# Kernel optimization log

Measured on AMD Instinct MI355X. Metric: run time of the kernel, lower is better.

Reference implementation:

```python
import math
import jax, jax.numpy as jnp
import numpy as np

B, T, C, HS = 4, 4096, 2048, 128

def setup_inputs() -> dict:
    key = jax.random.key(0)
    k1, k2, k3, k4 = jax.random.split(key, 4)
    x = jax.random.normal(k1, (B, T, C), dtype=jnp.float32)
    # torch Linear init ~ U(-1/sqrt(in), 1/sqrt(in)); normal*0.02 is fine for a numeric baseline
    Wq = jax.random.normal(k2, (C, HS), dtype=jnp.float32) * 0.02
    Wk = jax.random.normal(k3, (C, HS), dtype=jnp.float32) * 0.02
    Wv = jax.random.normal(k4, (C, HS), dtype=jnp.float32) * 0.02
    return {"x": x, "Wq": Wq, "Wk": Wk, "Wv": Wv}

def reference(x, Wq, Wk, Wv):
    # Single-head causal self-attention (dropout in eval mode = identity).
    q = x @ Wq          # [B,T,HS]
    k = x @ Wk          # [B,T,HS]
    v = x @ Wv          # [B,T,HS]
    scale = 1.0 / math.sqrt(HS)
    att = jnp.einsum('bqd,bkd->bqk', q, k) * scale          # [B,T,T]
    causal = jnp.tril(jnp.ones((T, T), dtype=bool))          # [T,T]
    att = jnp.where(causal[None, :, :], att, -jnp.inf)
    att = jax.nn.softmax(att, axis=-1)
    y = jnp.einsum('bqk,bkd->bqd', att, v)                   # [B,T,HS]
    return y
```

## Files before the change

### kernel.cpp

```cpp
#include <hip/hip_runtime.h>
#include <hip/hip_bf16.h>


#define B_  4
#define T_  4096
#define C_  2048
#define HS_ 128

typedef unsigned short u16;
typedef __attribute__((ext_vector_type(8))) short short8;
typedef __attribute__((ext_vector_type(4))) float floatx4;

static __device__ __forceinline__ u16 f2bf(float x) {
  union { float f; unsigned u; } c; c.f = x;
  unsigned r = 0x7fffu + ((c.u >> 16) & 1u);
  return (u16)((c.u + r) >> 16);
}

__global__ __launch_bounds__(256) void wtrans3_kernel(
    const float* __restrict__ Wq, const float* __restrict__ Wk,
    const float* __restrict__ Wv, u16* __restrict__ dst) {
  __shared__ u16 tile[32][33];
  int z = blockIdx.z;
  const float* src = (z == 0) ? Wq : (z == 1) ? Wk : Wv;
  u16* d = dst + (size_t)z * HS_ * C_;
  int c0 = blockIdx.x * 32, r0 = blockIdx.y * 32;
  int tx = threadIdx.x, ty = threadIdx.y;
#pragma unroll
  for (int i = 0; i < 4; ++i)
    tile[ty + 8 * i][tx] = f2bf(src[(size_t)(r0 + ty + 8 * i) * HS_ + (c0 + tx)]);
  __syncthreads();
#pragma unroll
  for (int i = 0; i < 4; ++i)
    d[(size_t)(c0 + ty + 8 * i) * C_ + (r0 + tx)] = tile[tx][ty + 8 * i];
}

#define GBM 64
#define GBK 64
#define LPAD 72

__global__ __launch_bounds__(256) void qkv_gemm_kernel(
    const float* __restrict__ X, const u16* __restrict__ WT3,
    u16* __restrict__ qkv, u16* __restrict__ vT) {
  __shared__ u16 smem[GBM * LPAD + HS_ * LPAD];
  u16 (*Xs)[LPAD] = (u16(*)[LPAD])smem;
  u16 (*Ws)[LPAD] = (u16(*)[LPAD])(smem + GBM * LPAD);

  int z = blockIdx.y;
  const u16* Wt = WT3 + (size_t)z * HS_ * C_;
  int t = threadIdx.x;
  int wv = t >> 6, lane = t & 63;
  int l15 = lane & 15, hi = lane >> 4;
  int wm = (wv & 1) * 32, wn = (wv >> 1) * 64;
  size_t mbase = (size_t)blockIdx.x * GBM;

  int xm = t >> 3, xc = t & 7;

  const float* xrow0 = &X[(mbase + xm) * C_];
  const float* xrow1 = &X[(mbase + 32 + xm) * C_];
  const u16* wrow0 = &Wt[(size_t)(xm) * C_];
  const u16* wrow1 = &Wt[(size_t)(32 + xm) * C_];
  const u16* wrow2 = &Wt[(size_t)(64 + xm) * C_];
  const u16* wrow3 = &Wt[(size_t)(96 + xm) * C_];

  floatx4 acc[2][4];
#pragma unroll
  for (int i = 0; i < 2; ++i)
#pragma unroll
    for (int j = 0; j < 4; ++j) acc[i][j] = (floatx4){0.f, 0.f, 0.f, 0.f};

  floatx4 xreg[2][2];
  short8 wreg[4];
  {
    int koff = xc * 8;
    xreg[0][0] = *(const floatx4*)&xrow0[koff];
    xreg[0][1] = *(const floatx4*)&xrow0[koff + 4];
    xreg[1][0] = *(const floatx4*)&xrow1[koff];
    xreg[1][1] = *(const floatx4*)&xrow1[koff + 4];
    wreg[0] = *(const short8*)&wrow0[koff];
    wreg[1] = *(const short8*)&wrow1[koff];
    wreg[2] = *(const short8*)&wrow2[koff];
    wreg[3] = *(const short8*)&wrow3[koff];
  }

  for (int kt = 0; kt < C_ / GBK; ++kt) {
#pragma unroll
    for (int i = 0; i < 2; ++i) {
      short8 v;
#pragma unroll
      for (int j = 0; j < 4; ++j) {
        v[j] = (short)f2bf(xreg[i][0][j]);
        v[4 + j] = (short)f2bf(xreg[i][1][j]);
      }
      *(short8*)&Xs[i * 32 + xm][xc * 8] = v;
    }
    *(short8*)&Ws[xm][xc * 8] = wreg[0];
    *(short8*)&Ws[32 + xm][xc * 8] = wreg[1];
    *(short8*)&Ws[64 + xm][xc * 8] = wreg[2];
    *(short8*)&Ws[96 + xm][xc * 8] = wreg[3];
    __syncthreads();

    if (kt + 1 < C_ / GBK) {
      int koff = (kt + 1) * GBK + xc * 8;
      xreg[0][0] = *(const floatx4*)&xrow0[koff];
      xreg[0][1] = *(const floatx4*)&xrow0[koff + 4];
      xreg[1][0] = *(const floatx4*)&xrow1[koff];
      xreg[1][1] = *(const floatx4*)&xrow1[koff + 4];
      wreg[0] = *(const short8*)&wrow0[koff];
      wreg[1] = *(const short8*)&wrow1[koff];
      wreg[2] = *(const short8*)&wrow2[koff];
      wreg[3] = *(const short8*)&wrow3[koff];
    }

#pragma unroll
    for (int ks = 0; ks < 2; ++ks) {
      short8 af[2], bf[4];
#pragma unroll
      for (int mt = 0; mt < 2; ++mt)
        af[mt] = *(const short8*)&Xs[wm + mt * 16 + l15][ks * 32 + hi * 8];
#pragma unroll
      for (int nt = 0; nt < 4; ++nt)
        bf[nt] = *(const short8*)&Ws[wn + nt * 16 + l15][ks * 32 + hi * 8];
#pragma unroll
      for (int mt = 0; mt < 2; ++mt)
#pragma unroll
        for (int nt = 0; nt < 4; ++nt)
          acc[mt][nt] = __builtin_amdgcn_mfma_f32_16x16x32_bf16(
              af[mt], bf[nt], acc[mt][nt], 0, 0, 0);
    }
    __syncthreads();
  }

  if (z != 2) {
    u16* outp = qkv + (size_t)z * ((size_t)B_ * T_ * HS_);
#pragma unroll
    for (int mt = 0; mt < 2; ++mt)
#pragma unroll
      for (int nt = 0; nt < 4; ++nt)
#pragma unroll
        for (int r = 0; r < 4; ++r) {
          size_t row = mbase + wm + mt * 16 + hi * 4 + r;
          int col = wn + nt * 16 + l15;
          outp[row * HS_ + col] = f2bf(acc[mt][nt][r]);
        }
  } else {
    u16 (*Tb)[LPAD] = (u16(*)[LPAD])smem;
#pragma unroll
    for (int mt = 0; mt < 2; ++mt)
#pragma unroll
      for (int nt = 0; nt < 4; ++nt)
#pragma unroll
        for (int r = 0; r < 4; ++r)
          Tb[wn + nt * 16 + l15][wm + mt * 16 + hi * 4 + r] = f2bf(acc[mt][nt][r]);
    __syncthreads();
    int b = (int)(mbase >> 12);
    int trow0 = (int)(mbase & (T_ - 1));
    u16* vb = vT + (size_t)b * HS_ * T_;
#pragma unroll
    for (int i = 0; i < 4; ++i) {
      int id = i * 256 + t;
      int c = id >> 3, ch = id & 7;
      short8 v = *(const short8*)&Tb[c][ch * 8];
      *(short8*)&vb[(size_t)c * T_ + trow0 + ch * 8] = v;
    }
  }
}

#define BQ 64
#define BKV 64
#define CHUNK 16

template <bool WRITE_PARTIAL>
static __device__ __forceinline__ void flash_body(
    const u16* __restrict__ q, const u16* __restrict__ k,
    const u16* __restrict__ vT, float* __restrict__ outO,
    float* __restrict__ Mp, float* __restrict__ Lp,
    int b, int qb, int kb0, int kb1, int slot) {
  __shared__ u16 Ks[BKV][136];
  __shared__ u16 Vs[144][72];
  __shared__ u16 Ps[BQ][72];
  int t = threadIdx.x;
  int wv = t >> 6, lane = t & 63, l15 = lane & 15, hi = lane >> 4;

  const float sc = 0.08838834764831845f * 1.4426950408889634f;

  short8 qf[4];
  {
    const u16* qrow = q + (size_t)(b * T_ + qb * BQ + wv * 16 + l15) * HS_;
#pragma unroll
    for (int ks = 0; ks < 4; ++ks)
      qf[ks] = *(const short8*)(qrow + ks * 32 + hi * 8);
  }

  {
    int r = 128 + (t >> 4), c0 = (t & 15) * 4;
    const u16 one = 0x3F80;
    Vs[r][c0] = one; Vs[r][c0 + 1] = one;
    Vs[r][c0 + 2] = one; Vs[r][c0 + 3] = one;
  }

  floatx4 of[9];
#pragma unroll
  for (int dt = 0; dt < 9; ++dt) of[dt] = (floatx4){0.f, 0.f, 0.f, 0.f};
  float m_run[4];
#pragma unroll
  for (int r = 0; r < 4; ++r) m_run[r] = -__builtin_inff();

  const u16* kbase = k + (size_t)b * T_ * HS_;
  const u16* vbase = vT + (size_t)b * HS_ * T_;

  short8 kreg[4], vreg[4];
#pragma unroll
  for (int i = 0; i < 4; ++i) {
    int id = i * 256 + t;
    int n = id >> 4, ck = id & 15;
    kreg[i] = *(const short8*)&kbase[(size_t)(kb0 * BKV + n) * HS_ + ck * 8];
    int d = id >> 3, cv = id & 7;
    vreg[i] = *(const short8*)&vbase[(size_t)d * T_ + kb0 * BKV + cv * 8];
  }

  for (int kb = kb0; kb <= kb1; ++kb) {
#pragma unroll
    for (int i = 0; i < 4; ++i) {
      int id = i * 256 + t;
      int n = id >> 4, ck = id & 15;
      *(short8*)&Ks[n][ck * 8] = kreg[i];
      int d = id >> 3, cv = id & 7;
      *(short8*)&Vs[d][cv * 8] = vreg[i];
    }
    __syncthreads();

    if (kb < kb1) {
#pragma unroll
      for (int i = 0; i < 4; ++i) {
        int id = i * 256 + t;
        int n = id >> 4, ck = id & 15;
        kreg[i] = *(const short8*)&kbase[(size_t)((kb + 1) * BKV + n) * HS_ + ck * 8];
        int d = id >> 3, cv = id & 7;
        vreg[i] = *(const short8*)&vbase[(size_t)d * T_ + (kb + 1) * BKV + cv * 8];
      }
    }

    floatx4 sf[4];
#pragma unroll
    for (int nt = 0; nt < 4; ++nt) {
      floatx4 s = (floatx4){0.f, 0.f, 0.f, 0.f};
#pragma unroll
      for (int ks = 0; ks < 4; ++ks) {
        short8 bfrag = *(const short8*)&Ks[nt * 16 + l15][ks * 32 + hi * 8];
        s = __builtin_amdgcn_mfma_f32_16x16x32_bf16(qf[ks], bfrag, s, 0, 0, 0);
      }
      sf[nt] = s;
    }

    float sv[4][4];
    if (kb == qb) {
#pragma unroll
      for (int nt = 0; nt < 4; ++nt) {
        int col = nt * 16 + l15;
#pragma unroll
        for (int r = 0; r < 4; ++r) {
          int row = wv * 16 + hi * 4 + r;
          sv[nt][r] = (col <= row) ? sf[nt][r] * sc : -__builtin_inff();
        }
      }
    } else {
#pragma unroll
      for (int nt = 0; nt < 4; ++nt)
#pragma unroll
        for (int r = 0; r < 4; ++r) sv[nt][r] = sf[nt][r] * sc;
    }

    float mt4[4];
#pragma unroll
    for (int r = 0; r < 4; ++r)
      mt4[r] = fmaxf(fmaxf(sv[0][r], sv[1][r]), fmaxf(sv[2][r], sv[3][r]));
#pragma unroll
    for (int off = 1; off < 16; off <<= 1)
#pragma unroll
      for (int r = 0; r < 4; ++r)
        mt4[r] = fmaxf(mt4[r], __shfl_xor(mt4[r], off));

    bool need = false;
#pragma unroll
    for (int r = 0; r < 4; ++r) need = need || (mt4[r] > m_run[r] + 8.f);
    if (__any(need)) {
      float alpha[4];
#pragma unroll
      for (int r = 0; r < 4; ++r) {
        float mn = fmaxf(m_run[r], mt4[r]);
        alpha[r] = exp2f(m_run[r] - mn);
        m_run[r] = mn;
      }
#pragma unroll
      for (int dt = 0; dt < 9; ++dt)
#pragma unroll
        for (int r = 0; r < 4; ++r) of[dt][r] *= alpha[r];
    }

    float pv[4][4];
#pragma unroll
    for (int nt = 0; nt < 4; ++nt)
#pragma unroll
      for (int r = 0; r < 4; ++r) pv[nt][r] = exp2f(sv[nt][r] - m_run[r]);

#pragma unroll
    for (int nt = 0; nt < 4; ++nt)
#pragma unroll
      for (int r = 0; r < 4; ++r)
        Ps[wv * 16 + hi * 4 + r][nt * 16 + l15] = f2bf(pv[nt][r]);
    __asm__ volatile("s_waitcnt lgkmcnt(0)" ::: "memory");

#pragma unroll
    for (int ks2 = 0; ks2 < 2; ++ks2) {
      short8 af = *(const short8*)&Ps[wv * 16 + l15][ks2 * 32 + hi * 8];
#pragma unroll
      for (int dt = 0; dt < 9; ++dt) {
        short8 bfrag = *(const short8*)&Vs[dt * 16 + l15][ks2 * 32 + hi * 8];
        of[dt] = __builtin_amdgcn_mfma_f32_16x16x32_bf16(af, bfrag, of[dt], 0, 0, 0);
      }
    }
    __syncthreads();
  }

  if (WRITE_PARTIAL) {
    float* Op = outO + (size_t)slot * (BQ * HS_);
#pragma unroll
    for (int dt = 0; dt < 8; ++dt)
#pragma unroll
      for (int r = 0; r < 4; ++r) {
        int row = wv * 16 + hi * 4 + r;
        Op[row * HS_ + dt * 16 + l15] = of[dt][r];
      }
    if (l15 == 0) {
#pragma unroll
      for (int r = 0; r < 4; ++r) {
        int row = wv * 16 + hi * 4 + r;
        Mp[slot * BQ + row] = m_run[r];
        Lp[slot * BQ + row] = of[8][r];
      }
    }
  } else {
    float rl[4];
#pragma unroll
    for (int r = 0; r < 4; ++r) rl[r] = 1.0f / of[8][r];
#pragma unroll
    for (int dt = 0; dt < 8; ++dt)
#pragma unroll
      for (int r = 0; r < 4; ++r) {
        size_t row = (size_t)(b * T_ + qb * BQ + wv * 16 + hi * 4 + r);
        outO[row * HS_ + dt * 16 + l15] = of[dt][r] * rl[r];
      }
  }
}

__global__ __launch_bounds__(256, 3) void flash_partial_kernel(
    const u16* __restrict__ q, const u16* __restrict__ k,
    const u16* __restrict__ vT, float* __restrict__ Opart,
    float* __restrict__ Mpart, float* __restrict__ Lpart) {
  int qb = blockIdx.x, c = blockIdx.y, b = blockIdx.z;
  int kb0 = c * CHUNK;
  if (kb0 > qb) return;
  int kb1 = min(qb, kb0 + CHUNK - 1);
  int slot = (b * (T_ / BQ) + qb) * 4 + c;
  flash_body<true>(q, k, vT, Opart, Mpart, Lpart, b, qb, kb0, kb1, slot);
}

__global__ __launch_bounds__(256, 3) void flash_attn_kernel(
    const u16* __restrict__ q, const u16* __restrict__ k,
    const u16* __restrict__ vT, float* __restrict__ out) {
  int qb = blockIdx.x, b = blockIdx.y;
  flash_body<false>(q, k, vT, out, nullptr, nullptr, b, qb, 0, qb, 0);
}

__global__ __launch_bounds__(256) void flash_merge_kernel(
    const float* __restrict__ Opart, const float* __restrict__ Mpart,
    const float* __restrict__ Lpart, float* __restrict__ out) {
  __shared__ float w[4][BQ];
  __shared__ float invL[BQ];
  int qb = blockIdx.x, b = blockIdx.y;
  int t = threadIdx.x;
  int nch = qb / CHUNK + 1;
  int slot0 = (b * (T_ / BQ) + qb) * 4;

  if (t < BQ) {
    float mv[4], mmax = -__builtin_inff();
    for (int c = 0; c < nch; ++c) {
      mv[c] = Mpart[(slot0 + c) * BQ + t];
      mmax = fmaxf(mmax, mv[c]);
    }
    float L = 0.f;
    for (int c = 0; c < nch; ++c) {
      float wc = exp2f(mv[c] - mmax);
      w[c][t] = wc;
      L += wc * Lpart[(slot0 + c) * BQ + t];
    }
    invL[t] = 1.0f / L;
  }
  __syncthreads();

  size_t obase = ((size_t)(b * T_) + (size_t)qb * BQ) * HS_;
#pragma unroll
  for (int j = 0; j < 32; ++j) {
    int e = j * 256 + t;
    int row = e >> 7;
    float acc = 0.f;
    for (int c = 0; c < nch; ++c)
      acc += w[c][row] * Opart[(size_t)(slot0 + c) * (BQ * HS_) + e];
    out[obase + e] = acc * invL[row];
  }
}

extern "C" void kernel_launch(void* const* d_in, const int* in_sizes, int n_in,
                              void* d_out, int out_size, void* d_ws, size_t ws_size,
                              hipStream_t stream) {
  const float* x  = (const float*)d_in[0];
  const float* Wq = (const float*)d_in[1];
  const float* Wk = (const float*)d_in[2];
  const float* Wv = (const float*)d_in[3];
  float* out = (float*)d_out;

  u16* ws = (u16*)d_ws;
  const size_t wtsz  = (size_t)HS_ * C_;
  const size_t qkvsz = (size_t)B_ * T_ * HS_;
  u16* WT = ws;
  u16* qv = WT + 3 * wtsz;
  u16* kv = qv + qkvsz;
  u16* vT = kv + qkvsz;
  const size_t base_bytes = (3 * wtsz + 3 * qkvsz) * sizeof(u16);

  const int NSLOT = B_ * (T_ / BQ) * 4;
  float* Opart = (float*)((char*)d_ws + base_bytes);
  float* Mpart = Opart + (size_t)NSLOT * BQ * HS_;
  float* Lpart = Mpart + (size_t)NSLOT * BQ;
  const size_t split_bytes =
      base_bytes + ((size_t)NSLOT * BQ * HS_ + 2 * (size_t)NSLOT * BQ) * sizeof(float);

  dim3 tb(32, 8);
  wtrans3_kernel<<<dim3(HS_ / 32, C_ / 32, 3), tb, 0, stream>>>(Wq, Wk, Wv, WT);

  qkv_gemm_kernel<<<dim3((B_ * T_) / GBM, 3), 256, 0, stream>>>(x, WT, qv, vT);

  if (ws_size >= split_bytes) {
    flash_partial_kernel<<<dim3(T_ / BQ, 4, B_), 256, 0, stream>>>(
        qv, kv, vT, Opart, Mpart, Lpart);
    flash_merge_kernel<<<dim3(T_ / BQ, B_), 256, 0, stream>>>(
        Opart, Mpart, Lpart, out);
  } else {
    flash_attn_kernel<<<dim3(T_ / BQ, B_), 256, 0, stream>>>(qv, kv, vT, out);
  }
}
```

Before: 306.9 us.

## Fuse Q/K/V projections into one GEMM block with double-buffered LDS

Measured after the change: 322.2 us. 5.0% more time.

```diff
diff --git a/kernel.cpp b/kernel.cpp
--- a/kernel.cpp
+++ b/kernel.cpp
@@ -37,128 +37,137 @@
 
 #define GBM 64
 #define GBK 64
-#define LPAD 72
-
-__global__ __launch_bounds__(256) void qkv_gemm_kernel(
+#define NKT (C_ / GBK)
+
+__global__ __launch_bounds__(512) void qkv_gemm_fused(
     const float* __restrict__ X, const u16* __restrict__ WT3,
     u16* __restrict__ qkv, u16* __restrict__ vT) {
-  __shared__ u16 smem[GBM * LPAD + HS_ * LPAD];
-  u16 (*Xs)[LPAD] = (u16(*)[LPAD])smem;
-  u16 (*Ws)[LPAD] = (u16(*)[LPAD])(smem + GBM * LPAD);
-
-  int z = blockIdx.y;
-  const u16* Wt = WT3 + (size_t)z * HS_ * C_;
+  __shared__ u16 Xs[2][GBM][72];
+  __shared__ u16 Ws[2][3 * HS_][72];
+
   int t = threadIdx.x;
   int wv = t >> 6, lane = t & 63;
   int l15 = lane & 15, hi = lane >> 4;
-  int wm = (wv & 1) * 32, wn = (wv >> 1) * 64;
+  int wm = (wv & 1) * 32;
+  int wn = (wv >> 1) * 32;
   size_t mbase = (size_t)blockIdx.x * GBM;
 
   int xm = t >> 3, xc = t & 7;
-
-  const float* xrow0 = &X[(mbase + xm) * C_];
-  const float* xrow1 = &X[(mbase + 32 + xm) * C_];
-  const u16* wrow0 = &Wt[(size_t)(xm) * C_];
-  const u16* wrow1 = &Wt[(size_t)(32 + xm) * C_];
-  const u16* wrow2 = &Wt[(size_t)(64 + xm) * C_];
-  const u16* wrow3 = &Wt[(size_t)(96 + xm) * C_];
-
-  floatx4 acc[2][4];
-#pragma unroll
-  for (int i = 0; i < 2; ++i)
-#pragma unroll
-    for (int j = 0; j < 4; ++j) acc[i][j] = (floatx4){0.f, 0.f, 0.f, 0.f};
-
-  floatx4 xreg[2][2];
-  short8 wreg[4];
+  const float* xrow = &X[(mbase + xm) * C_];
+  const u16* wb[6];
+#pragma unroll
+  for (int j = 0; j < 6; ++j) {
+    int g = xm + 64 * j;
+    wb[j] = &WT3[(size_t)(g >> 7) * HS_ * C_ + (size_t)(g & 127) * C_];
+  }
+
+  floatx4 acc[3][2][2];
+#pragma unroll
+  for (int z = 0; z < 3; ++z)
+#pragma unroll
+    for (int i = 0; i < 2; ++i)
+#pragma unroll
+      for (int j = 0; j < 2; ++j) acc[z][i][j] = (floatx4){0.f, 0.f, 0.f, 0.f};
+
+  floatx4 xreg[2];
+  short8 wreg[6];
+
   {
     int koff = xc * 8;
-    xreg[0][0] = *(const floatx4*)&xrow0[koff];
-    xreg[0][1] = *(const floatx4*)&xrow0[koff + 4];
-    xreg[1][0] = *(const floatx4*)&xrow1[koff];
-    xreg[1][1] = *(const floatx4*)&xrow1[koff + 4];
-    wreg[0] = *(const short8*)&wrow0[koff];
-    wreg[1] = *(const short8*)&wrow1[koff];
-    wreg[2] = *(const short8*)&wrow2[koff];
-    wreg[3] = *(const short8*)&wrow3[koff];
-  }
-
-  for (int kt = 0; kt < C_ / GBK; ++kt) {
-#pragma unroll
-    for (int i = 0; i < 2; ++i) {
-      short8 v;
+    xreg[0] = *(const floatx4*)&xrow[koff];
+    xreg[1] = *(const floatx4*)&xrow[koff + 4];
+#pragma unroll
+    for (int j = 0; j < 6; ++j) wreg[j] = *(const short8*)&wb[j][koff];
+  }
+  {
+    short8 xv;
+#pragma unroll
+    for (int j = 0; j < 4; ++j) {
+      xv[j] = (short)f2bf(xreg[0][j]);
+      xv[4 + j] = (short)f2bf(xreg[1][j]);
+    }
+    *(short8*)&Xs[0][xm][xc * 8] = xv;
+#pragma unroll
+    for (int j = 0; j < 6; ++j) *(short8*)&Ws[0][xm + 64 * j][xc * 8] = wreg[j];
+  }
+  __syncthreads();
+
+  for (int kt = 0; kt < NKT; ++kt) {
+    int p = kt & 1;
+    if (kt + 1 < NKT) {
+      int koff = (kt + 1) * GBK + xc * 8;
+      xreg[0] = *(const floatx4*)&xrow[koff];
+      xreg[1] = *(const floatx4*)&xrow[koff + 4];
+#pragma unroll
+      for (int j = 0; j < 6; ++j) wreg[j] = *(const short8*)&wb[j][koff];
+    }
+
+#pragma unroll
+    for (int ks = 0; ks < 2; ++ks) {
+      short8 af[2];
+#pragma unroll
+      for (int mt = 0; mt < 2; ++mt)
+        af[mt] = *(const short8*)&Xs[p][wm + mt * 16 + l15][ks * 32 + hi * 8];
+#pragma unroll
+      for (int z = 0; z < 3; ++z)
+#pragma unroll
+        for (int nt = 0; nt < 2; ++nt) {
+          short8 bfrag =
+              *(const short8*)&Ws[p][z * HS_ + wn + nt * 16 + l15][ks * 32 + hi * 8];
+#pragma unroll
+          for (int mt = 0; mt < 2; ++mt)
+            acc[z][mt][nt] = __builtin_amdgcn_mfma_f32_16x16x32_bf16(
+                af[mt], bfrag, acc[z][mt][nt], 0, 0, 0);
+        }
+    }
+
+    if (kt + 1 < NKT) {
+      short8 xv;
 #pragma unroll
       for (int j = 0; j < 4; ++j) {
-        v[j] = (short)f2bf(xreg[i][0][j]);
-        v[4 + j] = (short)f2bf(xreg[i][1][j]);
-      }
-      *(short8*)&Xs[i * 32 + xm][xc * 8] = v;
-    }
-    *(short8*)&Ws[xm][xc * 8] = wreg[0];
-    *(short8*)&Ws[32 + xm][xc * 8] = wreg[1];
-    *(short8*)&Ws[64 + xm][xc * 8] = wreg[2];
-    *(short8*)&Ws[96 + xm][xc * 8] = wreg[3];
+        xv[j] = (short)f2bf(xreg[0][j]);
+        xv[4 + j] = (short)f2bf(xreg[1][j]);
+      }
+      *(short8*)&Xs[p ^ 1][xm][xc * 8] = xv;
+#pragma unroll
+      for (int j = 0; j < 6; ++j)
+        *(short8*)&Ws[p ^ 1][xm + 64 * j][xc * 8] = wreg[j];
+    }
     __syncthreads();
-
-    if (kt + 1 < C_ / GBK) {
-      int koff = (kt + 1) * GBK + xc * 8;
-      xreg[0][0] = *(const floatx4*)&xrow0[koff];
-      xreg[0][1] = *(const floatx4*)&xrow0[koff + 4];
-      xreg[1][0] = *(const floatx4*)&xrow1[koff];
-      xreg[1][1] = *(const floatx4*)&xrow1[koff + 4];
-      wreg[0] = *(const short8*)&wrow0[koff];
-      wreg[1] = *(const short8*)&wrow1[koff];
-      wreg[2] = *(const short8*)&wrow2[koff];
-      wreg[3] = *(const short8*)&wrow3[koff];
-    }
-
-#pragma unroll
-    for (int ks = 0; ks < 2; ++ks) {
-      short8 af[2], bf[4];
-#pragma unroll
-      for (int mt = 0; mt < 2; ++mt)
-        af[mt] = *(const short8*)&Xs[wm + mt * 16 + l15][ks * 32 + hi * 8];
-#pragma unroll
-      for (int nt = 0; nt < 4; ++nt)
-        bf[nt] = *(const short8*)&Ws[wn + nt * 16 + l15][ks * 32 + hi * 8];
-#pragma unroll
-      for (int mt = 0; mt < 2; ++mt)
-#pragma unroll
-        for (int nt = 0; nt < 4; ++nt)
-          acc[mt][nt] = __builtin_amdgcn_mfma_f32_16x16x32_bf16(
-              af[mt], bf[nt], acc[mt][nt], 0, 0, 0);
-    }
-    __syncthreads();
-  }
-
-  if (z != 2) {
-    u16* outp = qkv + (size_t)z * ((size_t)B_ * T_ * HS_);
+  }
+
+  const size_t qkvsz = (size_t)B_ * T_ * HS_;
+#pragma unroll
+  for (int z = 0; z < 2; ++z) {
+    u16* outp = qkv + (size_t)z * qkvsz;
 #pragma unroll
     for (int mt = 0; mt < 2; ++mt)
 #pragma unroll
-      for (int nt = 0; nt < 4; ++nt)
+      for (int nt = 0; nt < 2; ++nt)
 #pragma unroll
         for (int r = 0; r < 4; ++r) {
           size_t row = mbase + wm + mt * 16 + hi * 4 + r;
           int col = wn + nt * 16 + l15;
-          outp[row * HS_ + col] = f2bf(acc[mt][nt][r]);
+          outp[row * HS_ + col] = f2bf(acc[z][mt][nt][r]);
         }
-  } else {
-    u16 (*Tb)[LPAD] = (u16(*)[LPAD])smem;
-#pragma unroll
-    for (int mt = 0; mt < 2; ++mt)
-#pragma unroll
-      for (int nt = 0; nt < 4; ++nt)
-#pragma unroll
-        for (int r = 0; r < 4; ++r)
-          Tb[wn + nt * 16 + l15][wm + mt * 16 + hi * 4 + r] = f2bf(acc[mt][nt][r]);
-    __syncthreads();
+  }
+
+  u16 (*Tb)[72] = (u16(*)[72])Ws[0];
+#pragma unroll
+  for (int mt = 0; mt < 2; ++mt)
+#pragma unroll
+    for (int nt = 0; nt < 2; ++nt)
+#pragma unroll
+      for (int r = 0; r < 4; ++r)
+        Tb[wn + nt * 16 + l15][wm + mt * 16 + hi * 4 + r] = f2bf(acc[2][mt][nt][r]);
+  __syncthreads();
+  {
     int b = (int)(mbase >> 12);
     int trow0 = (int)(mbase & (T_ - 1));
     u16* vb = vT + (size_t)b * HS_ * T_;
 #pragma unroll
-    for (int i = 0; i < 4; ++i) {
-      int id = i * 256 + t;
+    for (int i = 0; i < 2; ++i) {
+      int id = i * 512 + t;
       int c = id >> 3, ch = id & 7;
       short8 v = *(const short8*)&Tb[c][ch * 8];
       *(short8*)&vb[(size_t)c * T_ + trow0 + ch * 8] = v;
@@ -439,7 +448,7 @@
   dim3 tb(32, 8);
   wtrans3_kernel<<<dim3(HS_ / 32, C_ / 32, 3), tb, 0, stream>>>(Wq, Wk, Wv, WT);
 
-  qkv_gemm_kernel<<<dim3((B_ * T_) / GBM, 3), 256, 0, stream>>>(x, WT, qv, vT);
+  qkv_gemm_fused<<<dim3((B_ * T_) / GBM), 512, 0, stream>>>(x, WT, qv, vT);
 
   if (ws_size >= split_bytes) {
     flash_partial_kernel<<<dim3(T_ / BQ, 4, B_), 256, 0, stream>>>(
```

## Double-buffer LDS and enlarge QKV GEMM M-tile to 128 rows

Applied to the files above, without the earlier changes.

After: 322.2 us. 5.0% more time.

```diff
diff --git a/kernel.cpp b/kernel.cpp
--- a/kernel.cpp
+++ b/kernel.cpp
@@ -35,106 +35,117 @@
     d[(size_t)(c0 + ty + 8 * i) * C_ + (r0 + tx)] = tile[tx][ty + 8 * i];
 }
 
-#define GBM 64
+#define GBM 128
 #define GBK 64
-#define LPAD 72
-
-__global__ __launch_bounds__(256) void qkv_gemm_kernel(
+#define NKT (C_ / GBK)
+#define XP 72
+#define TP 136
+
+__global__ __launch_bounds__(256, 2) void qkv_gemm_kernel(
     const float* __restrict__ X, const u16* __restrict__ WT3,
     u16* __restrict__ qkv, u16* __restrict__ vT) {
-  __shared__ u16 smem[GBM * LPAD + HS_ * LPAD];
-  u16 (*Xs)[LPAD] = (u16(*)[LPAD])smem;
-  u16 (*Ws)[LPAD] = (u16(*)[LPAD])(smem + GBM * LPAD);
+  __shared__ u16 smem[2 * 2 * GBM * XP];
+  u16 (*Xs)[GBM][XP] = (u16(*)[GBM][XP])smem;
+  u16 (*Ws)[GBM][XP] = (u16(*)[GBM][XP])(smem + 2 * GBM * XP);
 
   int z = blockIdx.y;
   const u16* Wt = WT3 + (size_t)z * HS_ * C_;
   int t = threadIdx.x;
   int wv = t >> 6, lane = t & 63;
   int l15 = lane & 15, hi = lane >> 4;
-  int wm = (wv & 1) * 32, wn = (wv >> 1) * 64;
+  int wm = (wv & 1) * 64;
+  int wn = (wv >> 1) * 64;
   size_t mbase = (size_t)blockIdx.x * GBM;
 
-  int xm = t >> 3, xc = t & 7;
-
-  const float* xrow0 = &X[(mbase + xm) * C_];
-  const float* xrow1 = &X[(mbase + 32 + xm) * C_];
-  const u16* wrow0 = &Wt[(size_t)(xm) * C_];
-  const u16* wrow1 = &Wt[(size_t)(32 + xm) * C_];
-  const u16* wrow2 = &Wt[(size_t)(64 + xm) * C_];
-  const u16* wrow3 = &Wt[(size_t)(96 + xm) * C_];
-
-  floatx4 acc[2][4];
-#pragma unroll
-  for (int i = 0; i < 2; ++i)
+  int srow = t >> 3, sc = t & 7;
+  const float* xrowp[4];
+  const u16* wrowp[4];
+#pragma unroll
+  for (int i = 0; i < 4; ++i) {
+    xrowp[i] = &X[(mbase + i * 32 + srow) * C_];
+    wrowp[i] = &Wt[(size_t)(i * 32 + srow) * C_];
+  }
+
+  floatx4 acc[4][4];
+#pragma unroll
+  for (int i = 0; i < 4; ++i)
 #pragma unroll
     for (int j = 0; j < 4; ++j) acc[i][j] = (floatx4){0.f, 0.f, 0.f, 0.f};
 
-  floatx4 xreg[2][2];
+  floatx4 xreg[4][2];
   short8 wreg[4];
+
   {
-    int koff = xc * 8;
-    xreg[0][0] = *(const floatx4*)&xrow0[koff];
-    xreg[0][1] = *(const floatx4*)&xrow0[koff + 4];
-    xreg[1][0] = *(const floatx4*)&xrow1[koff];
-    xreg[1][1] = *(const floatx4*)&xrow1[koff + 4];
-    wreg[0] = *(const short8*)&wrow0[koff];
-    wreg[1] = *(const short8*)&wrow1[koff];
-    wreg[2] = *(const short8*)&wrow2[koff];
-    wreg[3] = *(const short8*)&wrow3[koff];
-  }
-
-  for (int kt = 0; kt < C_ / GBK; ++kt) {
-#pragma unroll
-    for (int i = 0; i < 2; ++i) {
-      short8 v;
-#pragma unroll
-      for (int j = 0; j < 4; ++j) {
-        v[j] = (short)f2bf(xreg[i][0][j]);
-        v[4 + j] = (short)f2bf(xreg[i][1][j]);
-      }
-      *(short8*)&Xs[i * 32 + xm][xc * 8] = v;
-    }
-    *(short8*)&Ws[xm][xc * 8] = wreg[0];
-    *(short8*)&Ws[32 + xm][xc * 8] = wreg[1];
-    *(short8*)&Ws[64 + xm][xc * 8] = wreg[2];
-    *(short8*)&Ws[96 + xm][xc * 8] = wreg[3];
-    __syncthreads();
-
-    if (kt + 1 < C_ / GBK) {
-      int koff = (kt + 1) * GBK + xc * 8;
-      xreg[0][0] = *(const floatx4*)&xrow0[koff];
-      xreg[0][1] = *(const floatx4*)&xrow0[koff + 4];
-      xreg[1][0] = *(const floatx4*)&xrow1[koff];
-      xreg[1][1] = *(const floatx4*)&xrow1[koff + 4];
-      wreg[0] = *(const short8*)&wrow0[koff];
-      wreg[1] = *(const short8*)&wrow1[koff];
-      wreg[2] = *(const short8*)&wrow2[koff];
-      wreg[3] = *(const short8*)&wrow3[koff];
+    int koff = sc * 8;
+#pragma unroll
+    for (int i = 0; i < 4; ++i) {
+      xreg[i][0] = *(const floatx4*)&xrowp[i][koff];
+      xreg[i][1] = *(const floatx4*)&xrowp[i][koff + 4];
+      wreg[i] = *(const short8*)&wrowp[i][koff];
+    }
+  }
+#pragma unroll
+  for (int i = 0; i < 4; ++i) {
+    short8 xv;
+#pragma unroll
+    for (int j = 0; j < 4; ++j) {
+      xv[j] = (short)f2bf(xreg[i][0][j]);
+      xv[4 + j] = (short)f2bf(xreg[i][1][j]);
+    }
+    *(short8*)&Xs[0][i * 32 + srow][sc * 8] = xv;
+    *(short8*)&Ws[0][i * 32 + srow][sc * 8] = wreg[i];
+  }
+  __syncthreads();
+
+  for (int kt = 0; kt < NKT; ++kt) {
+    int p = kt & 1;
+    if (kt + 1 < NKT) {
+      int koff = (kt + 1) * GBK + sc * 8;
+#pragma unroll
+      for (int i = 0; i < 4; ++i) {
+        xreg[i][0] = *(const floatx4*)&xrowp[i][koff];
+        xreg[i][1] = *(const floatx4*)&xrowp[i][koff + 4];
+        wreg[i] = *(const short8*)&wrowp[i][koff];
+      }
     }
 
 #pragma unroll
     for (int ks = 0; ks < 2; ++ks) {
-      short8 af[2], bf[4];
-#pragma unroll
-      for (int mt = 0; mt < 2; ++mt)
-        af[mt] = *(const short8*)&Xs[wm + mt * 16 + l15][ks * 32 + hi * 8];
+      short8 af[4], bf[4];
+#pragma unroll
+      for (int mt = 0; mt < 4; ++mt)
+        af[mt] = *(const short8*)&Xs[p][wm + mt * 16 + l15][ks * 32 + hi * 8];
 #pragma unroll
       for (int nt = 0; nt < 4; ++nt)
-        bf[nt] = *(const short8*)&Ws[wn + nt * 16 + l15][ks * 32 + hi * 8];
-#pragma unroll
-      for (int mt = 0; mt < 2; ++mt)
+        bf[nt] = *(const short8*)&Ws[p][wn + nt * 16 + l15][ks * 32 + hi * 8];
+#pragma unroll
+      for (int mt = 0; mt < 4; ++mt)
 #pragma unroll
         for (int nt = 0; nt < 4; ++nt)
           acc[mt][nt] = __builtin_amdgcn_mfma_f32_16x16x32_bf16(
               af[mt], bf[nt], acc[mt][nt], 0, 0, 0);
     }
+
+    if (kt + 1 < NKT) {
+#pragma unroll
+      for (int i = 0; i < 4; ++i) {
+        short8 xv;
+#pragma unroll
+        for (int j = 0; j < 4; ++j) {
+          xv[j] = (short)f2bf(xreg[i][0][j]);
+          xv[4 + j] = (short)f2bf(xreg[i][1][j]);
+        }
+        *(short8*)&Xs[p ^ 1][i * 32 + srow][sc * 8] = xv;
+        *(short8*)&Ws[p ^ 1][i * 32 + srow][sc * 8] = wreg[i];
+      }
+    }
     __syncthreads();
   }
 
   if (z != 2) {
     u16* outp = qkv + (size_t)z * ((size_t)B_ * T_ * HS_);
 #pragma unroll
-    for (int mt = 0; mt < 2; ++mt)
+    for (int mt = 0; mt < 4; ++mt)
 #pragma unroll
       for (int nt = 0; nt < 4; ++nt)
 #pragma unroll
@@ -144,9 +155,9 @@
           outp[row * HS_ + col] = f2bf(acc[mt][nt][r]);
         }
   } else {
-    u16 (*Tb)[LPAD] = (u16(*)[LPAD])smem;
-#pragma unroll
-    for (int mt = 0; mt < 2; ++mt)
+    u16 (*Tb)[TP] = (u16(*)[TP])smem;
+#pragma unroll
+    for (int mt = 0; mt < 4; ++mt)
 #pragma unroll
       for (int nt = 0; nt < 4; ++nt)
 #pragma unroll
@@ -157,9 +168,9 @@
     int trow0 = (int)(mbase & (T_ - 1));
     u16* vb = vT + (size_t)b * HS_ * T_;
 #pragma unroll
-    for (int i = 0; i < 4; ++i) {
+    for (int i = 0; i < 8; ++i) {
       int id = i * 256 + t;
-      int c = id >> 3, ch = id & 7;
+      int c = id >> 4, ch = id & 15;
       short8 v = *(const short8*)&Tb[c][ch * 8];
       *(short8*)&vb[(size_t)c * T_ + trow0 + ch * 8] = v;
     }
```
